# Performance work log

Measured on AMD Instinct MI355X. Metric: run time of the kernel, lower is better.

Reference implementation:

```python
import jax, jax.numpy as jnp
import numpy as np

N_NODES = 100_000
N_EDGES = 1_250_000
IN_CH = 64
HID = 64
OUT_CH = 10
K = 5
NUM_GRAPHS = 64


def setup_inputs() -> dict:
    key = jax.random.key(0)
    ks = jax.random.split(key, 8)
    x = jax.random.normal(ks[0], (N_NODES, IN_CH), dtype=jnp.float32)
    edge_index = jax.random.randint(ks[1], (2, N_EDGES), 0, N_NODES)
    batch = jnp.sort(jax.random.randint(ks[2], (N_NODES,), 0, NUM_GRAPHS))
    s_in = float(1.0 / np.sqrt(IN_CH))
    s_h = float(1.0 / np.sqrt(HID))
    W1 = jax.random.uniform(ks[3], (K, IN_CH, HID), minval=-s_in, maxval=s_in, dtype=jnp.float32)
    b1 = jnp.zeros((HID,), jnp.float32)
    W2 = jax.random.uniform(ks[4], (K, HID, HID), minval=-s_h, maxval=s_h, dtype=jnp.float32)
    b2 = jnp.zeros((HID,), jnp.float32)
    Wfc = jax.random.uniform(ks[5], (HID, OUT_CH), minval=-s_h, maxval=s_h, dtype=jnp.float32)
    bfc = jnp.zeros((OUT_CH,), jnp.float32)
    return dict(x=x, edge_index=edge_index, batch=batch,
                W1=W1, b1=b1, W2=W2, b2=b2, Wfc=Wfc, bfc=bfc)


def _cheb_conv(x, src, dst, W, b):
    """PyG ChebConv with normalization='rw', lambda_max=2.
    L_rw = I - D^{-1} A ; scaled L_hat = 2*L/lambda_max - I = -D^{-1}A
    (self-loop weights cancel to 0), so each hop is a weighted scatter-add."""
    n = x.shape[0]
    deg = jax.ops.segment_sum(jnp.ones((src.shape[0],), x.dtype), src, num_segments=n)
    inv_deg = jnp.where(deg > 0, 1.0 / deg, 0.0)
    ew = -inv_deg[src]  # per-edge weight of L_hat

    def prop(t):  # (L_hat t)[i] = sum_{j->i} ew * t[j]
        return jax.ops.segment_sum(ew[:, None] * t[src], dst, num_segments=n)

    Tx0 = x
    out = Tx0 @ W[0]
    Tx1 = prop(Tx0)
    out = out + Tx1 @ W[1]
    for k in range(2, W.shape[0]):
        Tx2 = 2.0 * prop(Tx1) - Tx0
        out = out + Tx2 @ W[k]
        Tx0, Tx1 = Tx1, Tx2
    return out + b


def reference(x, edge_index, batch, W1, b1, W2, b2, Wfc, bfc):
    src, dst = edge_index[0], edge_index[1]
    h = jax.nn.selu(_cheb_conv(x, src, dst, W1, b1))
    # AlphaDropout is identity at inference
    h = jax.nn.selu(_cheb_conv(h, src, dst, W2, b2))
    g = jax.ops.segment_sum(h, batch, num_segments=NUM_GRAPHS)  # global_add_pool
    return g @ Wfc + bfc
```

## Files before the change

### kernel.cpp

```cpp
#include <hip/hip_runtime.h>
#include <cstdint>

#define CH 64
#define POOL_NODES 256
#define NBLK 256
#define NBMAX 1024

typedef __attribute__((ext_vector_type(8))) short bf16x8;
typedef __attribute__((ext_vector_type(8))) unsigned short u16x8;
typedef __attribute__((ext_vector_type(4))) float f32x4;
typedef unsigned int uint32;

__device__ __forceinline__ unsigned short f2bf(float x) {
  unsigned u = __float_as_uint(x);
  u += 0x7FFF + ((u >> 16) & 1);
  return (unsigned short)(u >> 16);
}
__device__ __forceinline__ float bf2f(unsigned short h) {
  return __uint_as_float(((unsigned)h) << 16);
}
__device__ __forceinline__ float bflo(uint32 u) { return __uint_as_float(u << 16); }
__device__ __forceinline__ float bfhi(uint32 u) { return __uint_as_float(u & 0xFFFF0000u); }
__device__ __forceinline__ uint32 bfpack(float lo, float hi) {
  return ((uint32)f2bf(hi) << 16) | (uint32)f2bf(lo);
}

__global__ __launch_bounds__(256) void k_b1(const int* __restrict__ src, const int* __restrict__ dst,
                                            int* __restrict__ cntD, int* __restrict__ cntS, int E, int NB) {
  __shared__ int hD[NBMAX], hS[NBMAX];
  int t = threadIdx.x, b = blockIdx.x;
  for (int i = t; i < NBMAX; i += 256) { hD[i] = 0; hS[i] = 0; }
  __syncthreads();
  int chunk = (E + NBLK - 1) / NBLK;
  int e0 = b * chunk, e1 = min(E, e0 + chunk);
  for (int e = e0 + t; e < e1; e += 256) {
    atomicAdd(&hD[dst[e] >> 7], 1);
    atomicAdd(&hS[src[e] >> 7], 1);
  }
  __syncthreads();
  for (int i = t; i < NB; i += 256) {
    cntD[i * NBLK + b] = hD[i];
    cntS[i * NBLK + b] = hS[i];
  }
}

__global__ __launch_bounds__(256) void k_scan_local(const int* __restrict__ in, int* __restrict__ out,
                                                    int* __restrict__ bsum, int total) {
  __shared__ int s[256];
  int t = threadIdx.x;
  int base = blockIdx.x * 1024 + t * 4;
  int v0 = (base + 0 < total) ? in[base + 0] : 0;
  int v1 = (base + 1 < total) ? in[base + 1] : 0;
  int v2 = (base + 2 < total) ? in[base + 2] : 0;
  int v3 = (base + 3 < total) ? in[base + 3] : 0;
  int sum = v0 + v1 + v2 + v3;
  s[t] = sum;
  __syncthreads();
  for (int off = 1; off < 256; off <<= 1) {
    int x = (t >= off) ? s[t - off] : 0;
    __syncthreads();
    s[t] += x;
    __syncthreads();
  }
  int excl = s[t] - sum;
  if (base + 0 < total) out[base + 0] = excl;  excl += v0;
  if (base + 1 < total) out[base + 1] = excl;  excl += v1;
  if (base + 2 < total) out[base + 2] = excl;  excl += v2;
  if (base + 3 < total) out[base + 3] = excl;
  if (t == 255) bsum[blockIdx.x] = s[255];
}

__global__ __launch_bounds__(256) void k_scan_bsums(int* bsum, int nb) {
  __shared__ int s[256];
  int t = threadIdx.x;
  int v = (t < nb) ? bsum[t] : 0;
  s[t] = v;
  __syncthreads();
  for (int off = 1; off < 256; off <<= 1) {
    int x = (t >= off) ? s[t - off] : 0;
    __syncthreads();
    s[t] += x;
    __syncthreads();
  }
  if (t < nb) bsum[t] = s[t] - v;
}

__global__ __launch_bounds__(256) void k_scan_add(int* __restrict__ arr, const int* __restrict__ bsum, int total) {
  int i = blockIdx.x * 256 + threadIdx.x;
  if (i < total) arr[i] += bsum[i >> 10];
}

__global__ __launch_bounds__(256) void k_b2(const int* __restrict__ src, const int* __restrict__ dst,
                                            const int* __restrict__ cbaseD, const int* __restrict__ cbaseS,
                                            int2* __restrict__ erec_tmp, int* __restrict__ svals, int E, int NB) {
  __shared__ int curD[NBMAX], curS[NBMAX];
  int t = threadIdx.x, b = blockIdx.x;
  for (int i = t; i < NB; i += 256) {
    curD[i] = cbaseD[i * NBLK + b];
    curS[i] = cbaseS[i * NBLK + b];
  }
  __syncthreads();
  int chunk = (E + NBLK - 1) / NBLK;
  int e0 = b * chunk, e1 = min(E, e0 + chunk);
  for (int e = e0 + t; e < e1; e += 256) {
    int s = src[e], d = dst[e];
    int pd = atomicAdd(&curD[d >> 7], 1);
    erec_tmp[pd] = make_int2(s, d);
    int ps = atomicAdd(&curS[s >> 7], 1);
    svals[ps] = s;
  }
}

__global__ __launch_bounds__(256) void k_b3_deg(const int* __restrict__ svals, const int* __restrict__ cbaseS,
                                                float* __restrict__ neg_inv, int n, int E, int NB) {
  __shared__ int h[128];
  int t = threadIdx.x, k = blockIdx.x;
  if (t < 128) h[t] = 0;
  __syncthreads();
  int lo = cbaseS[k * NBLK];
  int hi = (k + 1 < NB) ? cbaseS[(k + 1) * NBLK] : E;
  for (int e = lo + t; e < hi; e += 256) atomicAdd(&h[svals[e] & 127], 1);
  __syncthreads();
  if (t < 128) {
    int node = k * 128 + t;
    if (node < n) {
      int c = h[t];
      neg_inv[node] = c > 0 ? (-1.0f / (float)c) : 0.0f;
    }
  }
}

__global__ __launch_bounds__(256) void k_b3_dst(const int2* __restrict__ erec_tmp, const int* __restrict__ cbaseD,
                                                const float* __restrict__ neg_inv, int2* __restrict__ erec,
                                                int* __restrict__ row_ptr, int n, int E, int NB) {
  __shared__ int h[128], sc[128], cur[128];
  int t = threadIdx.x, k = blockIdx.x;
  if (t < 128) h[t] = 0;
  __syncthreads();
  int lo = cbaseD[k * NBLK];
  int hi = (k + 1 < NB) ? cbaseD[(k + 1) * NBLK] : E;
  for (int e = lo + t; e < hi; e += 256) atomicAdd(&h[erec_tmp[e].y & 127], 1);
  __syncthreads();
  if (t < 128) sc[t] = h[t];
  __syncthreads();
  for (int off = 1; off < 128; off <<= 1) {
    int x = (t < 128 && t >= off) ? sc[t - off] : 0;
    __syncthreads();
    if (t < 128) sc[t] += x;
    __syncthreads();
  }
  if (t < 128) {
    int excl = sc[t] - h[t];
    cur[t] = excl;
    int node = k * 128 + t;
    if (node < n) row_ptr[node] = lo + excl;
  }
  if (k == NB - 1 && t == 0) row_ptr[n] = E;
  __syncthreads();
  for (int e = lo + t; e < hi; e += 256) {
    int2 r = erec_tmp[e];
    int pos = atomicAdd(&cur[r.y & 127], 1);
    erec[lo + pos] = make_int2(r.x, __float_as_int(neg_inv[r.x]));
  }
}

__global__ __launch_bounds__(256) void k_cast(const float* __restrict__ x, unsigned short* __restrict__ xb,
                                              int total8) {
  int i = blockIdx.x * 256 + threadIdx.x;
  if (i < total8) {
    const float4* p = (const float4*)(x + (size_t)i * 8);
    float4 v0 = p[0], v1 = p[1];
    u16x8 w;
    w[0] = f2bf(v0.x); w[1] = f2bf(v0.y); w[2] = f2bf(v0.z); w[3] = f2bf(v0.w);
    w[4] = f2bf(v1.x); w[5] = f2bf(v1.y); w[6] = f2bf(v1.z); w[7] = f2bf(v1.w);
    *(u16x8*)(xb + (size_t)i * 8) = w;
  }
}

__global__ __launch_bounds__(256) void k_prop(const int* __restrict__ row_ptr, const int2* __restrict__ erec,
                                              const uint32* __restrict__ t_in,
                                              const uint32* __restrict__ t_sub,
                                              uint32* __restrict__ t_out, int n, int mode) {
  int tid = threadIdx.x;
  int lane = tid & 63;
  int cp = lane & 31;
  int h = lane >> 5;
  int node = blockIdx.x * 8 + ((tid >> 6) << 1) + h;
  bool active = node < n;
  int beg = active ? row_ptr[node] : 0;
  int end = active ? row_ptr[node + 1] : 0;
  float a0 = 0.f, a1 = 0.f, b0 = 0.f, b1 = 0.f, c0 = 0.f, c1 = 0.f, d0 = 0.f, d1 = 0.f;
  float e0a = 0.f, e1a = 0.f, f0 = 0.f, f1 = 0.f, g0 = 0.f, g1 = 0.f, h0 = 0.f, h1 = 0.f;
  int e = beg;
  for (; e + 8 <= end; e += 8) {
    int2 q0 = erec[e + 0]; int2 q1 = erec[e + 1]; int2 q2 = erec[e + 2]; int2 q3 = erec[e + 3];
    int2 q4 = erec[e + 4]; int2 q5 = erec[e + 5]; int2 q6 = erec[e + 6]; int2 q7 = erec[e + 7];
    uint32 u0 = t_in[q0.x * 32 + cp];
    uint32 u1 = t_in[q1.x * 32 + cp];
    uint32 u2 = t_in[q2.x * 32 + cp];
    uint32 u3 = t_in[q3.x * 32 + cp];
    uint32 u4 = t_in[q4.x * 32 + cp];
    uint32 u5 = t_in[q5.x * 32 + cp];
    uint32 u6 = t_in[q6.x * 32 + cp];
    uint32 u7 = t_in[q7.x * 32 + cp];
    float w0 = __int_as_float(q0.y), w1 = __int_as_float(q1.y);
    float w2 = __int_as_float(q2.y), w3 = __int_as_float(q3.y);
    float w4 = __int_as_float(q4.y), w5 = __int_as_float(q5.y);
    float w6 = __int_as_float(q6.y), w7 = __int_as_float(q7.y);
    a0 = fmaf(w0, bflo(u0), a0);   a1 = fmaf(w0, bfhi(u0), a1);
    b0 = fmaf(w1, bflo(u1), b0);   b1 = fmaf(w1, bfhi(u1), b1);
    c0 = fmaf(w2, bflo(u2), c0);   c1 = fmaf(w2, bfhi(u2), c1);
    d0 = fmaf(w3, bflo(u3), d0);   d1 = fmaf(w3, bfhi(u3), d1);
    e0a = fmaf(w4, bflo(u4), e0a); e1a = fmaf(w4, bfhi(u4), e1a);
    f0 = fmaf(w5, bflo(u5), f0);   f1 = fmaf(w5, bfhi(u5), f1);
    g0 = fmaf(w6, bflo(u6), g0);   g1 = fmaf(w6, bfhi(u6), g1);
    h0 = fmaf(w7, bflo(u7), h0);   h1 = fmaf(w7, bfhi(u7), h1);
  }
  if (e + 4 <= end) {
    int2 q0 = erec[e + 0]; int2 q1 = erec[e + 1]; int2 q2 = erec[e + 2]; int2 q3 = erec[e + 3];
    uint32 u0 = t_in[q0.x * 32 + cp];
    uint32 u1 = t_in[q1.x * 32 + cp];
    uint32 u2 = t_in[q2.x * 32 + cp];
    uint32 u3 = t_in[q3.x * 32 + cp];
    float w0 = __int_as_float(q0.y), w1 = __int_as_float(q1.y);
    float w2 = __int_as_float(q2.y), w3 = __int_as_float(q3.y);
    a0 = fmaf(w0, bflo(u0), a0);   a1 = fmaf(w0, bfhi(u0), a1);
    b0 = fmaf(w1, bflo(u1), b0);   b1 = fmaf(w1, bfhi(u1), b1);
    c0 = fmaf(w2, bflo(u2), c0);   c1 = fmaf(w2, bfhi(u2), c1);
    d0 = fmaf(w3, bflo(u3), d0);   d1 = fmaf(w3, bfhi(u3), d1);
    e += 4;
  }
  if (e + 2 <= end) {
    int2 q0 = erec[e + 0]; int2 q1 = erec[e + 1];
    uint32 u0 = t_in[q0.x * 32 + cp];
    uint32 u1 = t_in[q1.x * 32 + cp];
    float w0 = __int_as_float(q0.y), w1 = __int_as_float(q1.y);
    a0 = fmaf(w0, bflo(u0), a0);   a1 = fmaf(w0, bfhi(u0), a1);
    b0 = fmaf(w1, bflo(u1), b0);   b1 = fmaf(w1, bfhi(u1), b1);
    e += 2;
  }
  if (e < end) {
    int2 q = erec[e];
    uint32 u = t_in[q.x * 32 + cp];
    float w = __int_as_float(q.y);
    a0 = fmaf(w, bflo(u), a0);
    a1 = fmaf(w, bfhi(u), a1);
  }
  float s0 = ((a0 + b0) + (c0 + d0)) + ((e0a + f0) + (g0 + h0));
  float s1 = ((a1 + b1) + (c1 + d1)) + ((e1a + f1) + (g1 + h1));
  if (active) {
    if (mode == 2) {
      uint32 u = t_sub[(size_t)node * 32 + cp];
      s0 = 2.0f * s0 - bflo(u);
      s1 = 2.0f * s1 - bfhi(u);
    }
    t_out[(size_t)node * 32 + cp] = bfpack(s0, s1);
  }
}

__global__ __launch_bounds__(256) void k_prepW(const float* __restrict__ W, unsigned short* __restrict__ Wt) {
  int o = blockIdx.x * 256 + threadIdx.x;
  if (o < 64 * 320) {
    int j = o / 320, k = o - j * 320;
    Wt[o] = f2bf(W[k * 64 + j]);
  }
}

template <typename OutT>
__global__ __launch_bounds__(256) void k_gemm5(
    const unsigned short* __restrict__ M0, const unsigned short* __restrict__ M1,
    const unsigned short* __restrict__ M2, const unsigned short* __restrict__ M3,
    const unsigned short* __restrict__ M4,
    const unsigned short* __restrict__ Wt, const float* __restrict__ bias,
    OutT* __restrict__ outp, int n) {
  __shared__ unsigned short lds[64 * 320];
  const int t = threadIdx.x;
  const int lane = t & 63, wave = t >> 6;
  const int node0 = blockIdx.x * 64;
  const unsigned short* mats[5] = {M0, M1, M2, M3, M4};
#pragma unroll
  for (int m = 0; m < 5; ++m) {
    const unsigned short* __restrict__ T = mats[m];
#pragma unroll
    for (int i = 0; i < 2; ++i) {
      int flat = i * 256 + t;
      int row = flat >> 3;
      int cc = flat & 7;
      int ca = m * 8 + cc;
      u16x8 w = {};
      if (node0 + row < n)
        w = *(const u16x8*)(T + (size_t)(node0 + row) * CH + cc * 8);
      *(u16x8*)(&lds[row * 320 + ((ca ^ (row & 7)) << 3)]) = w;
    }
  }
  __syncthreads();
  const int wr = wave >> 1, wc = wave & 1;
  const int g = lane >> 4, r16 = lane & 15;
  const int rowA0 = wr * 32 + r16, rowA1 = rowA0 + 16;
  const int colB0 = wc * 32 + r16, colB1 = colB0 + 16;
  f32x4 acc00 = {}, acc01 = {}, acc10 = {}, acc11 = {};
#pragma unroll 2
  for (int kk = 0; kk < 10; ++kk) {
    int ca = kk * 4 + g;
    bf16x8 a0 = *(const bf16x8*)(&lds[rowA0 * 320 + ((ca ^ (rowA0 & 7)) << 3)]);
    bf16x8 a1 = *(const bf16x8*)(&lds[rowA1 * 320 + ((ca ^ (rowA1 & 7)) << 3)]);
    bf16x8 b0 = *(const bf16x8*)(Wt + colB0 * 320 + kk * 32 + g * 8);
    bf16x8 b1 = *(const bf16x8*)(Wt + colB1 * 320 + kk * 32 + g * 8);
    acc00 = __builtin_amdgcn_mfma_f32_16x16x32_bf16(a0, b0, acc00, 0, 0, 0);
    acc01 = __builtin_amdgcn_mfma_f32_16x16x32_bf16(a0, b1, acc01, 0, 0, 0);
    acc10 = __builtin_amdgcn_mfma_f32_16x16x32_bf16(a1, b0, acc10, 0, 0, 0);
    acc11 = __builtin_amdgcn_mfma_f32_16x16x32_bf16(a1, b1, acc11, 0, 0, 0);
  }
  const float sc = 1.0507009873554805f, al = 1.6732632423543773f;
  const f32x4 accs[2][2] = {{acc00, acc01}, {acc10, acc11}};
#pragma unroll
  for (int i = 0; i < 2; ++i) {
#pragma unroll
    for (int j = 0; j < 2; ++j) {
      int col = wc * 32 + j * 16 + r16;
      float bv = bias[col];
#pragma unroll
      for (int rr = 0; rr < 4; ++rr) {
        int row = node0 + wr * 32 + i * 16 + g * 4 + rr;
        if (row < n) {
          float v = accs[i][j][rr] + bv;
          v = (v > 0.f) ? (sc * v) : (sc * al * (expf(v) - 1.f));
          if constexpr (sizeof(OutT) == 4) outp[(size_t)row * CH + col] = (OutT)v;
          else outp[(size_t)row * CH + col] = (OutT)f2bf(v);
        }
      }
    }
  }
}

__global__ __launch_bounds__(256) void k_pool(const float* __restrict__ h, const int* __restrict__ batch,
                                              float* __restrict__ g, int n) {
  int c = threadIdx.x & 63;
  int rg = threadIdx.x >> 6;
  int start = blockIdx.x * POOL_NODES;
  float cur = 0.f;
  int curg = -1;
  for (int j = rg; j < POOL_NODES; j += 4) {
    int i = start + j;
    if (i >= n) break;
    int b = batch[i];
    if (b != curg) {
      if (curg >= 0) atomicAdd(&g[curg * CH + c], cur);
      curg = b;
      cur = 0.f;
    }
    cur += h[(size_t)i * CH + c];
  }
  if (curg >= 0) atomicAdd(&g[curg * CH + c], cur);
}

__global__ __launch_bounds__(256) void k_fc(const float* __restrict__ g, const float* __restrict__ Wfc,
                                            const float* __restrict__ bfc, float* __restrict__ outp,
                                            int ng, int oc) {
  int i = blockIdx.x * 256 + threadIdx.x;
  if (i < ng * oc) {
    int gi = i / oc, o = i - gi * oc;
    float s = bfc[o];
    for (int ci = 0; ci < CH; ++ci) s += g[gi * CH + ci] * Wfc[ci * oc + o];
    outp[i] = s;
  }
}

extern "C" void kernel_launch(void* const* d_in, const int* in_sizes, int n_in,
                              void* d_out, int out_size, void* d_ws, size_t ws_size,
                              hipStream_t stream) {
  const float* x   = (const float*)d_in[0];
  const int* eidx  = (const int*)d_in[1];
  const int* batch = (const int*)d_in[2];
  const float* W1  = (const float*)d_in[3];
  const float* b1  = (const float*)d_in[4];
  const float* W2  = (const float*)d_in[5];
  const float* b2  = (const float*)d_in[6];
  const float* Wfc = (const float*)d_in[7];
  const float* bfc = (const float*)d_in[8];
  float* out = (float*)d_out;

  const int n  = in_sizes[0] / CH;
  const int E  = in_sizes[1] / 2;
  const int OC = in_sizes[8];
  const int NG = out_size / OC;
  const int NB = (n + 127) >> 7;

  const int* src = eidx;
  const int* dst = eidx + E;

  size_t off = 0;
  char* base = (char*)d_ws;
  auto alloc = [&](size_t bytes) -> void* {
    size_t cur = (off + 255) & ~(size_t)255;
    off = cur + bytes;
    return (void*)(base + cur);
  };
  const int scan_total = NB * NBLK;
  const int scan_nb    = (scan_total + 1023) / 1024;
  int*   cntD   = (int*)alloc((size_t)scan_total * 4);
  int*   cntS   = (int*)alloc((size_t)scan_total * 4);
  int*   bsumD  = (int*)alloc((size_t)scan_nb * 4);
  int*   bsumS  = (int*)alloc((size_t)scan_nb * 4);
  float* neg_inv = (float*)alloc((size_t)n * 4);
  int*   row_ptr = (int*)alloc((size_t)(n + 1) * 4);
  int2*  erec    = (int2*)alloc((size_t)E * 8);
  const size_t tb16 = (size_t)n * CH * 2;
  unsigned short* Xb = (unsigned short*)alloc(tb16);
  unsigned short* T1 = (unsigned short*)alloc(tb16);
  unsigned short* T2 = (unsigned short*)alloc(tb16);
  unsigned short* T3 = (unsigned short*)alloc(tb16);
  unsigned short* T4 = (unsigned short*)alloc(tb16);
  unsigned short* H  = (unsigned short*)alloc(tb16);
  float* H2 = (float*)alloc((size_t)n * CH * 4);
  float* g  = (float*)alloc((size_t)NG * CH * 4);
  unsigned short* Wt1 = (unsigned short*)alloc(64 * 320 * 2);
  unsigned short* Wt2 = (unsigned short*)alloc(64 * 320 * 2);
  if (off > ws_size) return;

  int2* erec_tmp = (int2*)H2;
  int*  svals    = (int*)(erec_tmp + E);

  hipMemsetAsync(g, 0, (size_t)NG * CH * 4, stream);

  k_b1<<<NBLK, 256, 0, stream>>>(src, dst, cntD, cntS, E, NB);
  k_scan_local<<<scan_nb, 256, 0, stream>>>(cntD, cntD, bsumD, scan_total);
  k_scan_bsums<<<1, 256, 0, stream>>>(bsumD, scan_nb);
  k_scan_add<<<(scan_total + 255) / 256, 256, 0, stream>>>(cntD, bsumD, scan_total);
  k_scan_local<<<scan_nb, 256, 0, stream>>>(cntS, cntS, bsumS, scan_total);
  k_scan_bsums<<<1, 256, 0, stream>>>(bsumS, scan_nb);
  k_scan_add<<<(scan_total + 255) / 256, 256, 0, stream>>>(cntS, bsumS, scan_total);
  k_b2<<<NBLK, 256, 0, stream>>>(src, dst, cntD, cntS, erec_tmp, svals, E, NB);
  k_b3_deg<<<NB, 256, 0, stream>>>(svals, cntS, neg_inv, n, E, NB);
  k_b3_dst<<<NB, 256, 0, stream>>>(erec_tmp, cntD, neg_inv, erec, row_ptr, n, E, NB);

  k_prepW<<<80, 256, 0, stream>>>(W1, Wt1);
  k_prepW<<<80, 256, 0, stream>>>(W2, Wt2);
  k_cast<<<(n * CH / 8 + 255) / 256, 256, 0, stream>>>(x, Xb, n * CH / 8);

  const int pb = (n + 7) / 8;
  const int gb = (n + 63) / 64;
  k_prop<<<pb, 256, 0, stream>>>(row_ptr, erec, (const uint32*)Xb, nullptr, (uint32*)T1, n, 1);
  k_prop<<<pb, 256, 0, stream>>>(row_ptr, erec, (const uint32*)T1, (const uint32*)Xb, (uint32*)T2, n, 2);
  k_prop<<<pb, 256, 0, stream>>>(row_ptr, erec, (const uint32*)T2, (const uint32*)T1, (uint32*)T3, n, 2);
  k_prop<<<pb, 256, 0, stream>>>(row_ptr, erec, (const uint32*)T3, (const uint32*)T2, (uint32*)T4, n, 2);
  k_gemm5<unsigned short><<<gb, 256, 0, stream>>>(Xb, T1, T2, T3, T4, Wt1, b1, H, n);
  k_prop<<<pb, 256, 0, stream>>>(row_ptr, erec, (const uint32*)H,  nullptr, (uint32*)T1, n, 1);
  k_prop<<<pb, 256, 0, stream>>>(row_ptr, erec, (const uint32*)T1, (const uint32*)H,  (uint32*)T2, n, 2);
  k_prop<<<pb, 256, 0, stream>>>(row_ptr, erec, (const uint32*)T2, (const uint32*)T1, (uint32*)T3, n, 2);
  k_prop<<<pb, 256, 0, stream>>>(row_ptr, erec, (const uint32*)T3, (const uint32*)T2, (uint32*)T4, n, 2);
  k_gemm5<float><<<gb, 256, 0, stream>>>(H, T1, T2, T3, T4, Wt2, b2, H2, n);
  k_pool<<<(n + POOL_NODES - 1) / POOL_NODES, 256, 0, stream>>>(H2, batch, g, n);
  k_fc<<<(NG * OC + 255) / 256, 256, 0, stream>>>(g, Wfc, bfc, out, NG, OC);
}
```

Baseline: 458.0 us.

## Pack edge records into 32-bit src+degree words and fuse second GEMM with pooling

Edge records shrink from an int2 (source index plus float weight) to one 32-bit word holding a 17-bit source index and a 15-bit clamped source degree. The weight is rebuilt in the propagation kernel with a hardware reciprocal, which halves edge-stream traffic and lets edges load as aligned 16-byte vectors after a short alignment prologue. The second GEMM now applies SELU, stages the result in LDS and does the global add-pool directly, removing the fp32 H2 write and readback and one kernel launch. The trade-offs are a node-count limit of 2^17, degree saturation at 32767, and approximate reciprocal precision.

```diff
diff --git a/kernel.cpp b/kernel.cpp
--- a/kernel.cpp
+++ b/kernel.cpp
@@ -2,9 +2,9 @@
 #include <cstdint>
 
 #define CH 64
-#define POOL_NODES 256
 #define NBLK 256
 #define NBMAX 1024
+#define SRCMASK 0x1FFFFu
 
 typedef __attribute__((ext_vector_type(8))) short bf16x8;
 typedef __attribute__((ext_vector_type(8))) unsigned short u16x8;
@@ -16,13 +16,13 @@
   u += 0x7FFF + ((u >> 16) & 1);
   return (unsigned short)(u >> 16);
 }
-__device__ __forceinline__ float bf2f(unsigned short h) {
-  return __uint_as_float(((unsigned)h) << 16);
-}
 __device__ __forceinline__ float bflo(uint32 u) { return __uint_as_float(u << 16); }
 __device__ __forceinline__ float bfhi(uint32 u) { return __uint_as_float(u & 0xFFFF0000u); }
 __device__ __forceinline__ uint32 bfpack(float lo, float hi) {
   return ((uint32)f2bf(hi) << 16) | (uint32)f2bf(lo);
+}
+__device__ __forceinline__ float recw(uint32 u) {
+  return __builtin_amdgcn_rcpf((float)(u >> 17));
 }
 
 __global__ __launch_bounds__(256) void k_b1(const int* __restrict__ src, const int* __restrict__ dst,
@@ -112,7 +112,7 @@
 }
 
 __global__ __launch_bounds__(256) void k_b3_deg(const int* __restrict__ svals, const int* __restrict__ cbaseS,
-                                                float* __restrict__ neg_inv, int n, int E, int NB) {
+                                                int* __restrict__ degv, int n, int E, int NB) {
   __shared__ int h[128];
   int t = threadIdx.x, k = blockIdx.x;
   if (t < 128) h[t] = 0;
@@ -123,15 +123,12 @@
   __syncthreads();
   if (t < 128) {
     int node = k * 128 + t;
-    if (node < n) {
-      int c = h[t];
-      neg_inv[node] = c > 0 ? (-1.0f / (float)c) : 0.0f;
-    }
+    if (node < n) degv[node] = h[t];
   }
 }
 
 __global__ __launch_bounds__(256) void k_b3_dst(const int2* __restrict__ erec_tmp, const int* __restrict__ cbaseD,
-                                                const float* __restrict__ neg_inv, int2* __restrict__ erec,
+                                                const int* __restrict__ degv, uint32* __restrict__ erec,
                                                 int* __restrict__ row_ptr, int n, int E, int NB) {
   __shared__ int h[128], sc[128], cur[128];
   int t = threadIdx.x, k = blockIdx.x;
@@ -160,7 +157,8 @@
   for (int e = lo + t; e < hi; e += 256) {
     int2 r = erec_tmp[e];
     int pos = atomicAdd(&cur[r.y & 127], 1);
-    erec[lo + pos] = make_int2(r.x, __float_as_int(neg_inv[r.x]));
+    uint32 d = (uint32)min(degv[r.x], 32767);
+    erec[lo + pos] = (d << 17) | (uint32)r.x;
   }
 }
 
@@ -177,7 +175,7 @@
   }
 }
 
-__global__ __launch_bounds__(256) void k_prop(const int* __restrict__ row_ptr, const int2* __restrict__ erec,
+__global__ __launch_bounds__(256) void k_prop(const int* __restrict__ row_ptr, const uint32* __restrict__ erec,
                                               const uint32* __restrict__ t_in,
                                               const uint32* __restrict__ t_sub,
                                               uint32* __restrict__ t_out, int n, int mode) {
@@ -192,59 +190,53 @@
   float a0 = 0.f, a1 = 0.f, b0 = 0.f, b1 = 0.f, c0 = 0.f, c1 = 0.f, d0 = 0.f, d1 = 0.f;
   float e0a = 0.f, e1a = 0.f, f0 = 0.f, f1 = 0.f, g0 = 0.f, g1 = 0.f, h0 = 0.f, h1 = 0.f;
   int e = beg;
+  int pre = min(end - e, (4 - (e & 3)) & 3);
+  for (int i = 0; i < pre; ++i, ++e) {
+    uint32 p = erec[e];
+    float w = recw(p);
+    uint32 u = t_in[(p & SRCMASK) * 32 + cp];
+    a0 = fmaf(-w, bflo(u), a0);  a1 = fmaf(-w, bfhi(u), a1);
+  }
   for (; e + 8 <= end; e += 8) {
-    int2 q0 = erec[e + 0]; int2 q1 = erec[e + 1]; int2 q2 = erec[e + 2]; int2 q3 = erec[e + 3];
-    int2 q4 = erec[e + 4]; int2 q5 = erec[e + 5]; int2 q6 = erec[e + 6]; int2 q7 = erec[e + 7];
-    uint32 u0 = t_in[q0.x * 32 + cp];
-    uint32 u1 = t_in[q1.x * 32 + cp];
-    uint32 u2 = t_in[q2.x * 32 + cp];
-    uint32 u3 = t_in[q3.x * 32 + cp];
-    uint32 u4 = t_in[q4.x * 32 + cp];
-    uint32 u5 = t_in[q5.x * 32 + cp];
-    uint32 u6 = t_in[q6.x * 32 + cp];
-    uint32 u7 = t_in[q7.x * 32 + cp];
-    float w0 = __int_as_float(q0.y), w1 = __int_as_float(q1.y);
-    float w2 = __int_as_float(q2.y), w3 = __int_as_float(q3.y);
-    float w4 = __int_as_float(q4.y), w5 = __int_as_float(q5.y);
-    float w6 = __int_as_float(q6.y), w7 = __int_as_float(q7.y);
-    a0 = fmaf(w0, bflo(u0), a0);   a1 = fmaf(w0, bfhi(u0), a1);
-    b0 = fmaf(w1, bflo(u1), b0);   b1 = fmaf(w1, bfhi(u1), b1);
-    c0 = fmaf(w2, bflo(u2), c0);   c1 = fmaf(w2, bfhi(u2), c1);
-    d0 = fmaf(w3, bflo(u3), d0);   d1 = fmaf(w3, bfhi(u3), d1);
-    e0a = fmaf(w4, bflo(u4), e0a); e1a = fmaf(w4, bfhi(u4), e1a);
-    f0 = fmaf(w5, bflo(u5), f0);   f1 = fmaf(w5, bfhi(u5), f1);
-    g0 = fmaf(w6, bflo(u6), g0);   g1 = fmaf(w6, bfhi(u6), g1);
-    h0 = fmaf(w7, bflo(u7), h0);   h1 = fmaf(w7, bfhi(u7), h1);
+    uint4 p0 = *(const uint4*)(erec + e);
+    uint4 p1 = *(const uint4*)(erec + e + 4);
+    uint32 u0 = t_in[(p0.x & SRCMASK) * 32 + cp];
+    uint32 u1 = t_in[(p0.y & SRCMASK) * 32 + cp];
+    uint32 u2 = t_in[(p0.z & SRCMASK) * 32 + cp];
+    uint32 u3 = t_in[(p0.w & SRCMASK) * 32 + cp];
+    uint32 u4 = t_in[(p1.x & SRCMASK) * 32 + cp];
+    uint32 u5 = t_in[(p1.y & SRCMASK) * 32 + cp];
+    uint32 u6 = t_in[(p1.z & SRCMASK) * 32 + cp];
+    uint32 u7 = t_in[(p1.w & SRCMASK) * 32 + cp];
+    float w0 = recw(p0.x), w1 = recw(p0.y), w2 = recw(p0.z), w3 = recw(p0.w);
+    float w4 = recw(p1.x), w5 = recw(p1.y), w6 = recw(p1.z), w7 = recw(p1.w);
+    a0 = fmaf(-w0, bflo(u0), a0);    a1 = fmaf(-w0, bfhi(u0), a1);
+    b0 = fmaf(-w1, bflo(u1), b0);    b1 = fmaf(-w1, bfhi(u1), b1);
+    c0 = fmaf(-w2, bflo(u2), c0);    c1 = fmaf(-w2, bfhi(u2), c1);
+    d0 = fmaf(-w3, bflo(u3), d0);    d1 = fmaf(-w3, bfhi(u3), d1);
+    e0a = fmaf(-w4, bflo(u4), e0a);  e1a = fmaf(-w4, bfhi(u4), e1a);
+    f0 = fmaf(-w5, bflo(u5), f0);    f1 = fmaf(-w5, bfhi(u5), f1);
+    g0 = fmaf(-w6, bflo(u6), g0);    g1 = fmaf(-w6, bfhi(u6), g1);
+    h0 = fmaf(-w7, bflo(u7), h0);    h1 = fmaf(-w7, bfhi(u7), h1);
   }
   if (e + 4 <= end) {
-    int2 q0 = erec[e + 0]; int2 q1 = erec[e + 1]; int2 q2 = erec[e + 2]; int2 q3 = erec[e + 3];
-    uint32 u0 = t_in[q0.x * 32 + cp];
-    uint32 u1 = t_in[q1.x * 32 + cp];
-    uint32 u2 = t_in[q2.x * 32 + cp];
-    uint32 u3 = t_in[q3.x * 32 + cp];
-    float w0 = __int_as_float(q0.y), w1 = __int_as_float(q1.y);
-    float w2 = __int_as_float(q2.y), w3 = __int_as_float(q3.y);
-    a0 = fmaf(w0, bflo(u0), a0);   a1 = fmaf(w0, bfhi(u0), a1);
-    b0 = fmaf(w1, bflo(u1), b0);   b1 = fmaf(w1, bfhi(u1), b1);
-    c0 = fmaf(w2, bflo(u2), c0);   c1 = fmaf(w2, bfhi(u2), c1);
-    d0 = fmaf(w3, bflo(u3), d0);   d1 = fmaf(w3, bfhi(u3), d1);
+    uint4 p0 = *(const uint4*)(erec + e);
+    uint32 u0 = t_in[(p0.x & SRCMASK) * 32 + cp];
+    uint32 u1 = t_in[(p0.y & SRCMASK) * 32 + cp];
+    uint32 u2 = t_in[(p0.z & SRCMASK) * 32 + cp];
+    uint32 u3 = t_in[(p0.w & SRCMASK) * 32 + cp];
+    float w0 = recw(p0.x), w1 = recw(p0.y), w2 = recw(p0.z), w3 = recw(p0.w);
+    a0 = fmaf(-w0, bflo(u0), a0);  a1 = fmaf(-w0, bfhi(u0), a1);
+    b0 = fmaf(-w1, bflo(u1), b0);  b1 = fmaf(-w1, bfhi(u1), b1);
+    c0 = fmaf(-w2, bflo(u2), c0);  c1 = fmaf(-w2, bfhi(u2), c1);
+    d0 = fmaf(-w3, bflo(u3), d0);  d1 = fmaf(-w3, bfhi(u3), d1);
     e += 4;
   }
-  if (e + 2 <= end) {
-    int2 q0 = erec[e + 0]; int2 q1 = erec[e + 1];
-    uint32 u0 = t_in[q0.x * 32 + cp];
-    uint32 u1 = t_in[q1.x * 32 + cp];
-    float w0 = __int_as_float(q0.y), w1 = __int_as_float(q1.y);
-    a0 = fmaf(w0, bflo(u0), a0);   a1 = fmaf(w0, bfhi(u0), a1);
-    b0 = fmaf(w1, bflo(u1), b0);   b1 = fmaf(w1, bfhi(u1), b1);
-    e += 2;
-  }
-  if (e < end) {
-    int2 q = erec[e];
-    uint32 u = t_in[q.x * 32 + cp];
-    float w = __int_as_float(q.y);
-    a0 = fmaf(w, bflo(u), a0);
-    a1 = fmaf(w, bfhi(u), a1);
+  for (; e < end; ++e) {
+    uint32 p = erec[e];
+    float w = recw(p);
+    uint32 u = t_in[(p & SRCMASK) * 32 + cp];
+    a0 = fmaf(-w, bflo(u), a0);  a1 = fmaf(-w, bfhi(u), a1);
   }
   float s0 = ((a0 + b0) + (c0 + d0)) + ((e0a + f0) + (g0 + h0));
   float s1 = ((a1 + b1) + (c1 + d1)) + ((e1a + f1) + (g1 + h1));
@@ -266,13 +258,17 @@
   }
 }
 
-template <typename OutT>
+__device__ __forceinline__ float selu(float v) {
+  const float sc = 1.0507009873554805f, al = 1.6732632423543773f;
+  return (v > 0.f) ? (sc * v) : (sc * al * (expf(v) - 1.f));
+}
+
 __global__ __launch_bounds__(256) void k_gemm5(
     const unsigned short* __restrict__ M0, const unsigned short* __restrict__ M1,
     const unsigned short* __restrict__ M2, const unsigned short* __restrict__ M3,
     const unsigned short* __restrict__ M4,
     const unsigned short* __restrict__ Wt, const float* __restrict__ bias,
-    OutT* __restrict__ outp, int n) {
+    unsigned short* __restrict__ outp, int n) {
   __shared__ unsigned short lds[64 * 320];
   const int t = threadIdx.x;
   const int lane = t & 63, wave = t >> 6;
@@ -311,7 +307,6 @@
     acc10 = __builtin_amdgcn_mfma_f32_16x16x32_bf16(a1, b0, acc10, 0, 0, 0);
     acc11 = __builtin_amdgcn_mfma_f32_16x16x32_bf16(a1, b1, acc11, 0, 0, 0);
   }
-  const float sc = 1.0507009873554805f, al = 1.6732632423543773f;
   const f32x4 accs[2][2] = {{acc00, acc01}, {acc10, acc11}};
 #pragma unroll
   for (int i = 0; i < 2; ++i) {
@@ -322,36 +317,90 @@
 #pragma unroll
       for (int rr = 0; rr < 4; ++rr) {
         int row = node0 + wr * 32 + i * 16 + g * 4 + rr;
-        if (row < n) {
-          float v = accs[i][j][rr] + bv;
-          v = (v > 0.f) ? (sc * v) : (sc * al * (expf(v) - 1.f));
-          if constexpr (sizeof(OutT) == 4) outp[(size_t)row * CH + col] = (OutT)v;
-          else outp[(size_t)row * CH + col] = (OutT)f2bf(v);
-        }
+        if (row < n)
+          outp[(size_t)row * CH + col] = f2bf(selu(accs[i][j][rr] + bv));
       }
     }
   }
 }
 
-__global__ __launch_bounds__(256) void k_pool(const float* __restrict__ h, const int* __restrict__ batch,
-                                              float* __restrict__ g, int n) {
-  int c = threadIdx.x & 63;
-  int rg = threadIdx.x >> 6;
-  int start = blockIdx.x * POOL_NODES;
+__global__ __launch_bounds__(256) void k_gemm5_pool(
+    const unsigned short* __restrict__ M0, const unsigned short* __restrict__ M1,
+    const unsigned short* __restrict__ M2, const unsigned short* __restrict__ M3,
+    const unsigned short* __restrict__ M4,
+    const unsigned short* __restrict__ Wt, const float* __restrict__ bias,
+    const int* __restrict__ batch, float* __restrict__ gout, int n) {
+  __shared__ unsigned short lds[64 * 320];
+  const int t = threadIdx.x;
+  const int lane = t & 63, wave = t >> 6;
+  const int node0 = blockIdx.x * 64;
+  const unsigned short* mats[5] = {M0, M1, M2, M3, M4};
+#pragma unroll
+  for (int m = 0; m < 5; ++m) {
+    const unsigned short* __restrict__ T = mats[m];
+#pragma unroll
+    for (int i = 0; i < 2; ++i) {
+      int flat = i * 256 + t;
+      int row = flat >> 3;
+      int cc = flat & 7;
+      int ca = m * 8 + cc;
+      u16x8 w = {};
+      if (node0 + row < n)
+        w = *(const u16x8*)(T + (size_t)(node0 + row) * CH + cc * 8);
+      *(u16x8*)(&lds[row * 320 + ((ca ^ (row & 7)) << 3)]) = w;
+    }
+  }
+  __syncthreads();
+  const int wr = wave >> 1, wc = wave & 1;
+  const int g = lane >> 4, r16 = lane & 15;
+  const int rowA0 = wr * 32 + r16, rowA1 = rowA0 + 16;
+  const int colB0 = wc * 32 + r16, colB1 = colB0 + 16;
+  f32x4 acc00 = {}, acc01 = {}, acc10 = {}, acc11 = {};
+#pragma unroll 2
+  for (int kk = 0; kk < 10; ++kk) {
+    int ca = kk * 4 + g;
+    bf16x8 a0 = *(const bf16x8*)(&lds[rowA0 * 320 + ((ca ^ (rowA0 & 7)) << 3)]);
+    bf16x8 a1 = *(const bf16x8*)(&lds[rowA1 * 320 + ((ca ^ (rowA1 & 7)) << 3)]);
+    bf16x8 b0 = *(const bf16x8*)(Wt + colB0 * 320 + kk * 32 + g * 8);
+    bf16x8 b1 = *(const bf16x8*)(Wt + colB1 * 320 + kk * 32 + g * 8);
+    acc00 = __builtin_amdgcn_mfma_f32_16x16x32_bf16(a0, b0, acc00, 0, 0, 0);
+    acc01 = __builtin_amdgcn_mfma_f32_16x16x32_bf16(a0, b1, acc01, 0, 0, 0);
+    acc10 = __builtin_amdgcn_mfma_f32_16x16x32_bf16(a1, b0, acc10, 0, 0, 0);
+    acc11 = __builtin_amdgcn_mfma_f32_16x16x32_bf16(a1, b1, acc11, 0, 0, 0);
+  }
+  __syncthreads();
+  float* S = (float*)lds;
+  const f32x4 accs[2][2] = {{acc00, acc01}, {acc10, acc11}};
+#pragma unroll
+  for (int i = 0; i < 2; ++i) {
+#pragma unroll
+    for (int j = 0; j < 2; ++j) {
+      int col = wc * 32 + j * 16 + r16;
+      float bv = bias[col];
+#pragma unroll
+      for (int rr = 0; rr < 4; ++rr) {
+        int row = wr * 32 + i * 16 + g * 4 + rr;
+        S[row * 65 + col] = selu(accs[i][j][rr] + bv);
+      }
+    }
+  }
+  __syncthreads();
+  int c = t & 63, w = t >> 6;
   float cur = 0.f;
   int curg = -1;
-  for (int j = rg; j < POOL_NODES; j += 4) {
-    int i = start + j;
-    if (i >= n) break;
-    int b = batch[i];
+  for (int r = 0; r < 16; ++r) {
+    int row = w * 16 + r;
+    int gn = node0 + row;
+    if (gn >= n) break;
+    int b = batch[gn];
     if (b != curg) {
-      if (curg >= 0) atomicAdd(&g[curg * CH + c], cur);
+      if (curg >= 0) atomicAdd(&gout[curg * CH + c], cur);
       curg = b;
       cur = 0.f;
     }
-    cur += h[(size_t)i * CH + c];
-  }
-  if (curg >= 0) atomicAdd(&g[curg * CH + c], cur);
+    cur += S[row * 65 + c];
+  }
+  if (curg >= 0) atomicAdd(&gout[curg * CH + c], cur);
 }
 
 __global__ __launch_bounds__(256) void k_fc(const float* __restrict__ g, const float* __restrict__ Wfc,
@@ -402,9 +451,9 @@
   int*   cntS   = (int*)alloc((size_t)scan_total * 4);
   int*   bsumD  = (int*)alloc((size_t)scan_nb * 4);
   int*   bsumS  = (int*)alloc((size_t)scan_nb * 4);
-  float* neg_inv = (float*)alloc((size_t)n * 4);
+  int*   degv    = (int*)alloc((size_t)n * 4);
   int*   row_ptr = (int*)alloc((size_t)(n + 1) * 4);
-  int2*  erec    = (int2*)alloc((size_t)E * 8);
+  uint32* erec   = (uint32*)alloc((size_t)E * 4);
   const size_t tb16 = (size_t)n * CH * 2;
   unsigned short* Xb = (unsigned short*)alloc(tb16);
   unsigned short* T1 = (unsigned short*)alloc(tb16);
@@ -412,13 +461,13 @@
   unsigned short* T3 = (unsigned short*)alloc(tb16);
   unsigned short* T4 = (unsigned short*)alloc(tb16);
   unsigned short* H  = (unsigned short*)alloc(tb16);
-  float* H2 = (float*)alloc((size_t)n * CH * 4);
+  char* scratch = (char*)alloc((size_t)E * 12);
   float* g  = (float*)alloc((size_t)NG * CH * 4);
   unsigned short* Wt1 = (unsigned short*)alloc(64 * 320 * 2);
   unsigned short* Wt2 = (unsigned short*)alloc(64 * 320 * 2);
   if (off > ws_size) return;
 
-  int2* erec_tmp = (int2*)H2;
+  int2* erec_tmp = (int2*)scratch;
   int*  svals    = (int*)(erec_tmp + E);
 
   hipMemsetAsync(g, 0, (size_t)NG * CH * 4, stream);
@@ -431,8 +480,8 @@
   k_scan_bsums<<<1, 256, 0, stream>>>(bsumS, scan_nb);
   k_scan_add<<<(scan_total + 255) / 256, 256, 0, stream>>>(cntS, bsumS, scan_total);
   k_b2<<<NBLK, 256, 0, stream>>>(src, dst, cntD, cntS, erec_tmp, svals, E, NB);
-  k_b3_deg<<<NB, 256, 0, stream>>>(svals, cntS, neg_inv, n, E, NB);
-  k_b3_dst<<<NB, 256, 0, stream>>>(erec_tmp, cntD, neg_inv, erec, row_ptr, n, E, NB);
+  k_b3_deg<<<NB, 256, 0, stream>>>(svals, cntS, degv, n, E, NB);
+  k_b3_dst<<<NB, 256, 0, stream>>>(erec_tmp, cntD, degv, erec, row_ptr, n, E, NB);
 
   k_prepW<<<80, 256, 0, stream>>>(W1, Wt1);
   k_prepW<<<80, 256, 0, stream>>>(W2, Wt2);
@@ -444,12 +493,11 @@
   k_prop<<<pb, 256, 0, stream>>>(row_ptr, erec, (const uint32*)T1, (const uint32*)Xb, (uint32*)T2, n, 2);
   k_prop<<<pb, 256, 0, stream>>>(row_ptr, erec, (const uint32*)T2, (const uint32*)T1, (uint32*)T3, n, 2);
   k_prop<<<pb, 256, 0, stream>>>(row_ptr, erec, (const uint32*)T3, (const uint32*)T2, (uint32*)T4, n, 2);
-  k_gemm5<unsigned short><<<gb, 256, 0, stream>>>(Xb, T1, T2, T3, T4, Wt1, b1, H, n);
+  k_gemm5<<<gb, 256, 0, stream>>>(Xb, T1, T2, T3, T4, Wt1, b1, H, n);
   k_prop<<<pb, 256, 0, stream>>>(row_ptr, erec, (const uint32*)H,  nullptr, (uint32*)T1, n, 1);
   k_prop<<<pb, 256, 0, stream>>>(row_ptr, erec, (const uint32*)T1, (const uint32*)H,  (uint32*)T2, n, 2);
   k_prop<<<pb, 256, 0, stream>>>(row_ptr, erec, (const uint32*)T2, (const uint32*)T1, (uint32*)T3, n, 2);
   k_prop<<<pb, 256, 0, stream>>>(row_ptr, erec, (const uint32*)T3, (const uint32*)T2, (uint32*)T4, n, 2);
-  k_gemm5<float><<<gb, 256, 0, stream>>>(H, T1, T2, T3, T4, Wt2, b2, H2, n);
-  k_pool<<<(n + POOL_NODES - 1) / POOL_NODES, 256, 0, stream>>>(H2, batch, g, n);
+  k_gemm5_pool<<<gb, 256, 0, stream>>>(H, T1, T2, T3, T4, Wt2, b2, batch, g, n);
   k_fc<<<(NG * OC + 255) / 256, 256, 0, stream>>>(g, Wfc, bfc, out, NG, OC);
 }
```

Result: slower. 490.9 us (+7.2%).

## Fuse second GEMM with global pooling and compact CSR build temporaries

Applied to the files above, without the earlier changes.

The second ChebConv GEMM now applies SELU, stages each 64-node tile in LDS and pools it straight into the per-graph sums with atomics. This removes the fp32 H2 write and the separate pool kernel's read. The CSR build also packs each temporary edge record into one 32-bit word (17-bit source, 7-bit local destination) and stores source degree keys as bytes, which cuts that traffic. The packing assumes node ids fit in 17 bits, and the fused kernel adds an extra LDS round trip and block barriers.

```diff
diff --git a/kernel.cpp b/kernel.cpp
--- a/kernel.cpp
+++ b/kernel.cpp
@@ -2,22 +2,20 @@
 #include <cstdint>
 
 #define CH 64
-#define POOL_NODES 256
 #define NBLK 256
 #define NBMAX 1024
+#define SRCMASK 0x1FFFFu
 
 typedef __attribute__((ext_vector_type(8))) short bf16x8;
 typedef __attribute__((ext_vector_type(8))) unsigned short u16x8;
 typedef __attribute__((ext_vector_type(4))) float f32x4;
 typedef unsigned int uint32;
+typedef unsigned char uchar;
 
 __device__ __forceinline__ unsigned short f2bf(float x) {
   unsigned u = __float_as_uint(x);
   u += 0x7FFF + ((u >> 16) & 1);
   return (unsigned short)(u >> 16);
-}
-__device__ __forceinline__ float bf2f(unsigned short h) {
-  return __uint_as_float(((unsigned)h) << 16);
 }
 __device__ __forceinline__ float bflo(uint32 u) { return __uint_as_float(u << 16); }
 __device__ __forceinline__ float bfhi(uint32 u) { return __uint_as_float(u & 0xFFFF0000u); }
@@ -92,7 +90,7 @@
 
 __global__ __launch_bounds__(256) void k_b2(const int* __restrict__ src, const int* __restrict__ dst,
                                             const int* __restrict__ cbaseD, const int* __restrict__ cbaseS,
-                                            int2* __restrict__ erec_tmp, int* __restrict__ svals, int E, int NB) {
+                                            uint32* __restrict__ etmp, uchar* __restrict__ svals, int E, int NB) {
   __shared__ int curD[NBMAX], curS[NBMAX];
   int t = threadIdx.x, b = blockIdx.x;
   for (int i = t; i < NB; i += 256) {
@@ -105,13 +103,13 @@
   for (int e = e0 + t; e < e1; e += 256) {
     int s = src[e], d = dst[e];
     int pd = atomicAdd(&curD[d >> 7], 1);
-    erec_tmp[pd] = make_int2(s, d);
+    etmp[pd] = ((uint32)(d & 127) << 17) | (uint32)s;
     int ps = atomicAdd(&curS[s >> 7], 1);
-    svals[ps] = s;
-  }
-}
-
-__global__ __launch_bounds__(256) void k_b3_deg(const int* __restrict__ svals, const int* __restrict__ cbaseS,
+    svals[ps] = (uchar)(s & 127);
+  }
+}
+
+__global__ __launch_bounds__(256) void k_b3_deg(const uchar* __restrict__ svals, const int* __restrict__ cbaseS,
                                                 float* __restrict__ neg_inv, int n, int E, int NB) {
   __shared__ int h[128];
   int t = threadIdx.x, k = blockIdx.x;
@@ -119,7 +117,7 @@
   __syncthreads();
   int lo = cbaseS[k * NBLK];
   int hi = (k + 1 < NB) ? cbaseS[(k + 1) * NBLK] : E;
-  for (int e = lo + t; e < hi; e += 256) atomicAdd(&h[svals[e] & 127], 1);
+  for (int e = lo + t; e < hi; e += 256) atomicAdd(&h[svals[e]], 1);
   __syncthreads();
   if (t < 128) {
     int node = k * 128 + t;
@@ -130,7 +128,7 @@
   }
 }
 
-__global__ __launch_bounds__(256) void k_b3_dst(const int2* __restrict__ erec_tmp, const int* __restrict__ cbaseD,
+__global__ __launch_bounds__(256) void k_b3_dst(const uint32* __restrict__ etmp, const int* __restrict__ cbaseD,
                                                 const float* __restrict__ neg_inv, int2* __restrict__ erec,
                                                 int* __restrict__ row_ptr, int n, int E, int NB) {
   __shared__ int h[128], sc[128], cur[128];
@@ -139,7 +137,7 @@
   __syncthreads();
   int lo = cbaseD[k * NBLK];
   int hi = (k + 1 < NB) ? cbaseD[(k + 1) * NBLK] : E;
-  for (int e = lo + t; e < hi; e += 256) atomicAdd(&h[erec_tmp[e].y & 127], 1);
+  for (int e = lo + t; e < hi; e += 256) atomicAdd(&h[(etmp[e] >> 17) & 127], 1);
   __syncthreads();
   if (t < 128) sc[t] = h[t];
   __syncthreads();
@@ -158,9 +156,10 @@
   if (k == NB - 1 && t == 0) row_ptr[n] = E;
   __syncthreads();
   for (int e = lo + t; e < hi; e += 256) {
-    int2 r = erec_tmp[e];
-    int pos = atomicAdd(&cur[r.y & 127], 1);
-    erec[lo + pos] = make_int2(r.x, __float_as_int(neg_inv[r.x]));
+    uint32 r = etmp[e];
+    int s = (int)(r & SRCMASK);
+    int pos = atomicAdd(&cur[(r >> 17) & 127], 1);
+    erec[lo + pos] = make_int2(s, __float_as_int(neg_inv[s]));
   }
 }
 
@@ -266,13 +265,17 @@
   }
 }
 
-template <typename OutT>
+__device__ __forceinline__ float selu(float v) {
+  const float sc = 1.0507009873554805f, al = 1.6732632423543773f;
+  return (v > 0.f) ? (sc * v) : (sc * al * (expf(v) - 1.f));
+}
+
 __global__ __launch_bounds__(256) void k_gemm5(
     const unsigned short* __restrict__ M0, const unsigned short* __restrict__ M1,
     const unsigned short* __restrict__ M2, const unsigned short* __restrict__ M3,
     const unsigned short* __restrict__ M4,
     const unsigned short* __restrict__ Wt, const float* __restrict__ bias,
-    OutT* __restrict__ outp, int n) {
+    unsigned short* __restrict__ outp, int n) {
   __shared__ unsigned short lds[64 * 320];
   const int t = threadIdx.x;
   const int lane = t & 63, wave = t >> 6;
@@ -311,7 +314,6 @@
     acc10 = __builtin_amdgcn_mfma_f32_16x16x32_bf16(a1, b0, acc10, 0, 0, 0);
     acc11 = __builtin_amdgcn_mfma_f32_16x16x32_bf16(a1, b1, acc11, 0, 0, 0);
   }
-  const float sc = 1.0507009873554805f, al = 1.6732632423543773f;
   const f32x4 accs[2][2] = {{acc00, acc01}, {acc10, acc11}};
 #pragma unroll
   for (int i = 0; i < 2; ++i) {
@@ -322,36 +324,90 @@
 #pragma unroll
       for (int rr = 0; rr < 4; ++rr) {
         int row = node0 + wr * 32 + i * 16 + g * 4 + rr;
-        if (row < n) {
-          float v = accs[i][j][rr] + bv;
-          v = (v > 0.f) ? (sc * v) : (sc * al * (expf(v) - 1.f));
-          if constexpr (sizeof(OutT) == 4) outp[(size_t)row * CH + col] = (OutT)v;
-          else outp[(size_t)row * CH + col] = (OutT)f2bf(v);
-        }
+        if (row < n)
+          outp[(size_t)row * CH + col] = f2bf(selu(accs[i][j][rr] + bv));
       }
     }
   }
 }
 
-__global__ __launch_bounds__(256) void k_pool(const float* __restrict__ h, const int* __restrict__ batch,
-                                              float* __restrict__ g, int n) {
-  int c = threadIdx.x & 63;
-  int rg = threadIdx.x >> 6;
-  int start = blockIdx.x * POOL_NODES;
+__global__ __launch_bounds__(256) void k_gemm5_pool(
+    const unsigned short* __restrict__ M0, const unsigned short* __restrict__ M1,
+    const unsigned short* __restrict__ M2, const unsigned short* __restrict__ M3,
+    const unsigned short* __restrict__ M4,
+    const unsigned short* __restrict__ Wt, const float* __restrict__ bias,
+    const int* __restrict__ batch, float* __restrict__ gout, int n) {
+  __shared__ unsigned short lds[64 * 320];
+  const int t = threadIdx.x;
+  const int lane = t & 63, wave = t >> 6;
+  const int node0 = blockIdx.x * 64;
+  const unsigned short* mats[5] = {M0, M1, M2, M3, M4};
+#pragma unroll
+  for (int m = 0; m < 5; ++m) {
+    const unsigned short* __restrict__ T = mats[m];
+#pragma unroll
+    for (int i = 0; i < 2; ++i) {
+      int flat = i * 256 + t;
+      int row = flat >> 3;
+      int cc = flat & 7;
+      int ca = m * 8 + cc;
+      u16x8 w = {};
+      if (node0 + row < n)
+        w = *(const u16x8*)(T + (size_t)(node0 + row) * CH + cc * 8);
+      *(u16x8*)(&lds[row * 320 + ((ca ^ (row & 7)) << 3)]) = w;
+    }
+  }
+  __syncthreads();
+  const int wr = wave >> 1, wc = wave & 1;
+  const int g = lane >> 4, r16 = lane & 15;
+  const int rowA0 = wr * 32 + r16, rowA1 = rowA0 + 16;
+  const int colB0 = wc * 32 + r16, colB1 = colB0 + 16;
+  f32x4 acc00 = {}, acc01 = {}, acc10 = {}, acc11 = {};
+#pragma unroll 2
+  for (int kk = 0; kk < 10; ++kk) {
+    int ca = kk * 4 + g;
+    bf16x8 a0 = *(const bf16x8*)(&lds[rowA0 * 320 + ((ca ^ (rowA0 & 7)) << 3)]);
+    bf16x8 a1 = *(const bf16x8*)(&lds[rowA1 * 320 + ((ca ^ (rowA1 & 7)) << 3)]);
+    bf16x8 b0 = *(const bf16x8*)(Wt + colB0 * 320 + kk * 32 + g * 8);
+    bf16x8 b1 = *(const bf16x8*)(Wt + colB1 * 320 + kk * 32 + g * 8);
+    acc00 = __builtin_amdgcn_mfma_f32_16x16x32_bf16(a0, b0, acc00, 0, 0, 0);
+    acc01 = __builtin_amdgcn_mfma_f32_16x16x32_bf16(a0, b1, acc01, 0, 0, 0);
+    acc10 = __builtin_amdgcn_mfma_f32_16x16x32_bf16(a1, b0, acc10, 0, 0, 0);
+    acc11 = __builtin_amdgcn_mfma_f32_16x16x32_bf16(a1, b1, acc11, 0, 0, 0);
+  }
+  __syncthreads();
+  float* S = (float*)lds;
+  const f32x4 accs[2][2] = {{acc00, acc01}, {acc10, acc11}};
+#pragma unroll
+  for (int i = 0; i < 2; ++i) {
+#pragma unroll
+    for (int j = 0; j < 2; ++j) {
+      int col = wc * 32 + j * 16 + r16;
+      float bv = bias[col];
+#pragma unroll
+      for (int rr = 0; rr < 4; ++rr) {
+        int row = wr * 32 + i * 16 + g * 4 + rr;
+        S[row * 65 + col] = selu(accs[i][j][rr] + bv);
+      }
+    }
+  }
+  __syncthreads();
+  int c = t & 63, w = t >> 6;
   float cur = 0.f;
   int curg = -1;
-  for (int j = rg; j < POOL_NODES; j += 4) {
-    int i = start + j;
-    if (i >= n) break;
-    int b = batch[i];
+  for (int r = 0; r < 16; ++r) {
+    int row = w * 16 + r;
+    int gn = node0 + row;
+    if (gn >= n) break;
+    int b = batch[gn];
     if (b != curg) {
-      if (curg >= 0) atomicAdd(&g[curg * CH + c], cur);
+      if (curg >= 0) atomicAdd(&gout[curg * CH + c], cur);
       curg = b;
       cur = 0.f;
     }
-    cur += h[(size_t)i * CH + c];
-  }
-  if (curg >= 0) atomicAdd(&g[curg * CH + c], cur);
+    cur += S[row * 65 + c];
+  }
+  if (curg >= 0) atomicAdd(&gout[curg * CH + c], cur);
 }
 
 __global__ __launch_bounds__(256) void k_fc(const float* __restrict__ g, const float* __restrict__ Wfc,
@@ -412,14 +468,12 @@
   unsigned short* T3 = (unsigned short*)alloc(tb16);
   unsigned short* T4 = (unsigned short*)alloc(tb16);
   unsigned short* H  = (unsigned short*)alloc(tb16);
-  float* H2 = (float*)alloc((size_t)n * CH * 4);
+  uint32* etmp  = (uint32*)alloc((size_t)E * 4);
+  uchar*  svals = (uchar*)alloc((size_t)E);
   float* g  = (float*)alloc((size_t)NG * CH * 4);
   unsigned short* Wt1 = (unsigned short*)alloc(64 * 320 * 2);
   unsigned short* Wt2 = (unsigned short*)alloc(64 * 320 * 2);
   if (off > ws_size) return;
-
-  int2* erec_tmp = (int2*)H2;
-  int*  svals    = (int*)(erec_tmp + E);
 
   hipMemsetAsync(g, 0, (size_t)NG * CH * 4, stream);
 
@@ -430,9 +484,9 @@
   k_scan_local<<<scan_nb, 256, 0, stream>>>(cntS, cntS, bsumS, scan_total);
   k_scan_bsums<<<1, 256, 0, stream>>>(bsumS, scan_nb);
   k_scan_add<<<(scan_total + 255) / 256, 256, 0, stream>>>(cntS, bsumS, scan_total);
-  k_b2<<<NBLK, 256, 0, stream>>>(src, dst, cntD, cntS, erec_tmp, svals, E, NB);
+  k_b2<<<NBLK, 256, 0, stream>>>(src, dst, cntD, cntS, etmp, svals, E, NB);
   k_b3_deg<<<NB, 256, 0, stream>>>(svals, cntS, neg_inv, n, E, NB);
-  k_b3_dst<<<NB, 256, 0, stream>>>(erec_tmp, cntD, neg_inv, erec, row_ptr, n, E, NB);
+  k_b3_dst<<<NB, 256, 0, stream>>>(etmp, cntD, neg_inv, erec, row_ptr, n, E, NB);
 
   k_prepW<<<80, 256, 0, stream>>>(W1, Wt1);
   k_prepW<<<80, 256, 0, stream>>>(W2, Wt2);
@@ -444,12 +498,11 @@
   k_prop<<<pb, 256, 0, stream>>>(row_ptr, erec, (const uint32*)T1, (const uint32*)Xb, (uint32*)T2, n, 2);
   k_prop<<<pb, 256, 0, stream>>>(row_ptr, erec, (const uint32*)T2, (const uint32*)T1, (uint32*)T3, n, 2);
   k_prop<<<pb, 256, 0, stream>>>(row_ptr, erec, (const uint32*)T3, (const uint32*)T2, (uint32*)T4, n, 2);
-  k_gemm5<unsigned short><<<gb, 256, 0, stream>>>(Xb, T1, T2, T3, T4, Wt1, b1, H, n);
+  k_gemm5<<<gb, 256, 0, stream>>>(Xb, T1, T2, T3, T4, Wt1, b1, H, n);
   k_prop<<<pb, 256, 0, stream>>>(row_ptr, erec, (const uint32*)H,  nullptr, (uint32*)T1, n, 1);
   k_prop<<<pb, 256, 0, stream>>>(row_ptr, erec, (const uint32*)T1, (const uint32*)H,  (uint32*)T2, n, 2);
   k_prop<<<pb, 256, 0, stream>>>(row_ptr, erec, (const uint32*)T2, (const uint32*)T1, (uint32*)T3, n, 2);
   k_prop<<<pb, 256, 0, stream>>>(row_ptr, erec, (const uint32*)T3, (const uint32*)T2, (uint32*)T4, n, 2);
-  k_gemm5<float><<<gb, 256, 0, stream>>>(H, T1, T2, T3, T4, Wt2, b2, H2, n);
-  k_pool<<<(n + POOL_NODES - 1) / POOL_NODES, 256, 0, stream>>>(H2, batch, g, n);
+  k_gemm5_pool<<<gb, 256, 0, stream>>>(H, T1, T2, T3, T4, Wt2, b2, batch, g, n);
   k_fc<<<(NG * OC + 255) / 256, 256, 0, stream>>>(g, Wfc, bfc, out, NG, OC);
 }
```

After: 421.6 us. -7.9%, faster.
